# Optimization experiments

Measured on AMD Instinct MI355X. Metric: run time of the kernel, lower is better.

## Reference

```python
import jax, jax.numpy as jnp
import numpy as np

N_NODES = 50000
N_EDGES = 800000
IN_FEATS = 96
H_FEATS = 256
N_HOPS = 3
N_NIE = N_HOPS + 1  # hops 0..3
NDIM_FC = N_NIE * H_FEATS


def setup_inputs() -> dict:
    key = jax.random.key(0)
    ks = jax.random.split(key, 8)
    edge_index = jax.random.randint(ks[0], (2, N_EDGES), 0, N_NODES, dtype=jnp.int64)
    features = jax.random.normal(ks[1], (N_NODES, IN_FEATS), dtype=jnp.float32)
    # per-hop MLP params: Linear(in_feats, h_feats) for each of n_nie hops
    s_in = 1.0 / np.sqrt(IN_FEATS)
    Ws = jax.random.uniform(ks[2], (N_NIE, IN_FEATS, H_FEATS), jnp.float32, -s_in, s_in)
    bs = jax.random.uniform(ks[3], (N_NIE, H_FEATS), jnp.float32, -s_in, s_in)
    # fusion: Linear(ndim_fc, h_feats)
    s_fc = 1.0 / np.sqrt(NDIM_FC)
    Wf = jax.random.uniform(ks[4], (NDIM_FC, H_FEATS), jnp.float32, -s_fc, s_fc)
    bf = jax.random.uniform(ks[5], (H_FEATS,), jnp.float32, -s_fc, s_fc)
    return {"edge_index": edge_index, "features": features, "Ws": Ws, "bs": bs, "Wf": Wf, "bf": bf}


def _build_norm_adj(edge_index):
    """set_diag (remove existing diag, add unit self-loops) + symmetric D^-1/2 A D^-1/2.
    Returns (rows, cols, edge_w) COO of the normalized adjacency."""
    row, col = edge_index[0].astype(jnp.int32), edge_index[1].astype(jnp.int32)
    loop = jnp.arange(N_NODES, dtype=jnp.int32)
    rows = jnp.concatenate([row, loop])
    cols = jnp.concatenate([col, loop])
    # zero out any pre-existing diagonal entries, self-loops get weight 1 (set_diag semantics)
    w = jnp.concatenate([(row != col).astype(jnp.float32), jnp.ones((N_NODES,), jnp.float32)])
    deg = jax.ops.segment_sum(w, rows, num_segments=N_NODES)
    dinv = jnp.where(deg > 0, jax.lax.rsqrt(deg), 0.0)
    edge_w = dinv[rows] * w * dinv[cols]
    return rows, cols, edge_w


def _spmm(rows, cols, edge_w, x):
    # out[r] = sum_e w_e * x[cols[e]] for edges with rows[e]==r
    return jax.ops.segment_sum(edge_w[:, None] * x[cols], rows, num_segments=N_NODES)


def reference(edge_index, features, Ws, bs, Wf, bf):
    rows, cols, edge_w = _build_norm_adj(edge_index)
    # row-normalize features (F.normalize dim=1)
    x = features / jnp.maximum(jnp.linalg.norm(features, axis=1, keepdims=True), 1e-12)
    nei_feats = [x]
    h = x
    for _ in range(N_HOPS):
        h = _spmm(rows, cols, edge_w, h)
        nei_feats.append(h)
    # per-hop MLP (dropout p=0 -> identity; norm=None -> identity) then ReLU
    ns = [jax.nn.relu(nei_feats[i] @ Ws[i] + bs[i]) for i in range(N_NIE)]
    cat = jnp.concatenate(ns, axis=1)  # [N, ndim_fc]
    out = jax.nn.relu(cat @ Wf + bf)   # [N, h_feats]
    return out
```

## Files before the change

kernel.cpp:

```cpp
#include <hip/hip_runtime.h>

#define N_NODES 50000
#define N_EDGES 800000
#define IN_F 96
#define H_F 256
#define N_NIE 4
#define SCAN_NB 196
#define BM 64
#define NBLK 782
#define LDA1 104
#define LDW 40

typedef float f32x4 __attribute__((ext_vector_type(4)));
typedef short s16x8 __attribute__((ext_vector_type(8)));
typedef unsigned short ushort;

__device__ __forceinline__ ushort bf16_rne(float f) {
    unsigned u = __float_as_uint(f);
    u += 0x7fffu + ((u >> 16) & 1u);
    return (ushort)(u >> 16);
}
__device__ __forceinline__ float bf16_f(ushort h) {
    return __uint_as_float(((unsigned)h) << 16);
}

__global__ __launch_bounds__(256) void k_count(const int* __restrict__ rows,
                                               const int* __restrict__ cols,
                                               int* __restrict__ cnt) {
    int i = blockIdx.x * 256 + threadIdx.x;
    if (i >= N_EDGES / 2) return;
    int2 r2 = ((const int2*)rows)[i];
    int2 c2 = ((const int2*)cols)[i];
    if (r2.x != c2.x) atomicAdd(&cnt[r2.x], 1);
    if (r2.y != c2.y) atomicAdd(&cnt[r2.y], 1);
}

__global__ __launch_bounds__(256) void k_scan1(const int* __restrict__ cnt,
                                               int* __restrict__ rowptr,
                                               int* __restrict__ bsum) {
    __shared__ int s[256];
    int t = threadIdx.x, e = blockIdx.x * 256 + t;
    int v = (e < N_NODES) ? cnt[e] : 0;
    s[t] = v;
    __syncthreads();
    #pragma unroll
    for (int off = 1; off < 256; off <<= 1) {
        int nv = (t >= off) ? s[t - off] : 0;
        __syncthreads();
        s[t] += nv;
        __syncthreads();
    }
    if (e < N_NODES) rowptr[e] = s[t] - v;
    if (t == 255) bsum[blockIdx.x] = s[255];
}

__global__ __launch_bounds__(256) void k_scan2(int* __restrict__ bsum,
                                               int* __restrict__ boff,
                                               int* __restrict__ rowptr) {
    __shared__ int s[256];
    int t = threadIdx.x;
    int v = (t < SCAN_NB) ? bsum[t] : 0;
    s[t] = v;
    __syncthreads();
    #pragma unroll
    for (int off = 1; off < 256; off <<= 1) {
        int nv = (t >= off) ? s[t - off] : 0;
        __syncthreads();
        s[t] += nv;
        __syncthreads();
    }
    if (t < SCAN_NB) boff[t] = s[t] - v;
    if (t == 255) rowptr[N_NODES] = s[255];
}

__global__ __launch_bounds__(256) void k_scan3(const int* __restrict__ boff,
                                               const int* __restrict__ cnt,
                                               int* __restrict__ rowptr,
                                               int* __restrict__ cursor,
                                               float* __restrict__ dinv) {
    int e = blockIdx.x * 256 + threadIdx.x;
    if (e >= N_NODES) return;
    int r = rowptr[e] + boff[blockIdx.x];
    rowptr[e] = r;
    cursor[e] = r;
    dinv[e] = rsqrtf((float)cnt[e] + 1.0f);
}

__global__ __launch_bounds__(256) void k_scatter(const int* __restrict__ rows,
                                                 const int* __restrict__ cols,
                                                 const float* __restrict__ dinv,
                                                 int* __restrict__ cursor,
                                                 int2* __restrict__ cw) {
    int e = blockIdx.x * 256 + threadIdx.x;
    if (e >= N_EDGES) return;
    int r = rows[e], c = cols[e];
    if (r == c) return;
    int p = atomicAdd(&cursor[r], 1);
    long long v = ((long long)(unsigned)__float_as_int(dinv[c]) << 32) | (unsigned)c;
    __builtin_nontemporal_store(v, (long long*)&cw[p]);
}

__global__ __launch_bounds__(256) void k_wsplit(const float* __restrict__ src,
                                                ushort* __restrict__ dh,
                                                int K, int N, int total) {
    int idx = blockIdx.x * 256 + threadIdx.x;
    if (idx >= total) return;
    int kn = K * N;
    int g = idx / kn, rem = idx - g * kn;
    int k = rem / N, n = rem - k * N;
    dh[g * kn + n * K + k] = bf16_rne(src[idx]);
}

__global__ __launch_bounds__(256) void k_norm(const float* __restrict__ feat,
                                              ushort* __restrict__ x) {
    int wid = (blockIdx.x * 256 + threadIdx.x) >> 6;
    int lane = threadIdx.x & 63;
    if (wid >= N_NODES) return;
    const float* fr = feat + (size_t)wid * IN_F;
    float v0 = (lane < IN_F) ? fr[lane] : 0.0f;
    float v1 = (lane < IN_F - 64) ? fr[64 + lane] : 0.0f;
    float ss = v0 * v0 + v1 * v1;
    #pragma unroll
    for (int o = 32; o; o >>= 1) ss += __shfl_xor(ss, o, 64);
    float inv = 1.0f / fmaxf(sqrtf(ss), 1e-12f);
    ushort* xr = x + (size_t)wid * IN_F;
    if (lane < IN_F) xr[lane] = bf16_rne(v0 * inv);
    if (lane < IN_F - 64) xr[64 + lane] = bf16_rne(v1 * inv);
}

__global__ __launch_bounds__(256) void k_spmm_csr(const int* __restrict__ rowptr,
                                                  const int2* __restrict__ cw,
                                                  const float* __restrict__ dinv,
                                                  const ushort* __restrict__ x,
                                                  ushort* __restrict__ y) {
    int g = (blockIdx.x * 256 + threadIdx.x) >> 5;
    if (g >= N_NODES) return;
    int l = threadIdx.x & 31;
    float dr = dinv[g];
    const ushort* xg = x + (size_t)g * IN_F;
    float s0 = bf16_f(xg[l]), s1 = bf16_f(xg[l + 32]), s2 = bf16_f(xg[l + 64]);
    float a0 = 0.f, a1 = 0.f, a2 = 0.f;
    float b0 = 0.f, b1 = 0.f, b2 = 0.f;
    float c0 = 0.f, c1 = 0.f, c2 = 0.f;
    float d0 = 0.f, d1 = 0.f, d2 = 0.f;
    int k = rowptr[g], e = rowptr[g + 1];
    for (; k + 3 < e; k += 4) {
        int2 p0 = cw[k], p1 = cw[k + 1], p2 = cw[k + 2], p3 = cw[k + 3];
        const ushort* x0 = x + (size_t)p0.x * IN_F;
        const ushort* x1 = x + (size_t)p1.x * IN_F;
        const ushort* x2 = x + (size_t)p2.x * IN_F;
        const ushort* x3 = x + (size_t)p3.x * IN_F;
        float w0 = __int_as_float(p0.y), w1 = __int_as_float(p1.y);
        float w2 = __int_as_float(p2.y), w3 = __int_as_float(p3.y);
        a0 += bf16_f(x0[l]) * w0; a1 += bf16_f(x0[l + 32]) * w0; a2 += bf16_f(x0[l + 64]) * w0;
        b0 += bf16_f(x1[l]) * w1; b1 += bf16_f(x1[l + 32]) * w1; b2 += bf16_f(x1[l + 64]) * w1;
        c0 += bf16_f(x2[l]) * w2; c1 += bf16_f(x2[l + 32]) * w2; c2 += bf16_f(x2[l + 64]) * w2;
        d0 += bf16_f(x3[l]) * w3; d1 += bf16_f(x3[l + 32]) * w3; d2 += bf16_f(x3[l + 64]) * w3;
    }
    for (; k < e; ++k) {
        int2 p0 = cw[k];
        float w0 = __int_as_float(p0.y);
        const ushort* x0 = x + (size_t)p0.x * IN_F;
        a0 += bf16_f(x0[l]) * w0; a1 += bf16_f(x0[l + 32]) * w0; a2 += bf16_f(x0[l + 64]) * w0;
    }
    ushort* yr = y + (size_t)g * IN_F;
    yr[l]      = bf16_rne(dr * ((a0 + b0) + (c0 + d0) + dr * s0));
    yr[l + 32] = bf16_rne(dr * ((a1 + b1) + (c1 + d1) + dr * s1));
    yr[l + 64] = bf16_rne(dr * ((a2 + b2) + (c2 + d2) + dr * s2));
}

__global__ __launch_bounds__(512, 4) void k_mega(const ushort* __restrict__ h0,
                                                 const ushort* __restrict__ h1,
                                                 const ushort* __restrict__ h2,
                                                 const ushort* __restrict__ h3,
                                                 const ushort* __restrict__ WsT,
                                                 const float* __restrict__ bs,
                                                 const ushort* __restrict__ WfT,
                                                 const float* __restrict__ bf,
                                                 float* __restrict__ out) {
    __shared__ ushort SM[36864];
    ushort* nsH = SM;
    ushort* Wb0 = SM + 16384;
    ushort* Wb1 = SM + 26624;
    ushort* Bs = Wb0;
    ushort* Ah = Wb1;
    float* T = (float*)SM;

    int m0 = blockIdx.x * BM;
    int tid = threadIdx.x;
    int lane = tid & 63, w = tid >> 6;
    int rsel = lane & 15, g = lane >> 4, ksel = g * 8;
    int crow = g * 4, ccol = rsel;
    int rw0 = (w & 3) * 16;
    int cwb = (w >> 2) * 32;

    int sr0 = tid / 12, sj0 = tid - sr0 * 12;
    int f1 = tid + 512;
    int sr1 = f1 / 12, sj1 = f1 - sr1 * 12;
    int wr_ = tid >> 2, wj_ = tid & 3;

    f32x4 acc[4][2] = {};

    for (int hop = 0; hop < N_NIE; ++hop) {
        const ushort* A = (hop == 0) ? h0 : (hop == 1) ? h1 : (hop == 2) ? h2 : h3;
        const ushort* wsT = WsT + hop * IN_F * H_F;
        const ushort* wfT = WfT + hop * H_F * H_F;
        const float* bsi = bs + hop * H_F;

        {
            int gm = m0 + sr0;
            s16x8 v = {0, 0, 0, 0, 0, 0, 0, 0};
            if (gm < N_NODES) v = *(const s16x8*)&A[(size_t)gm * IN_F + sj0 * 8];
            *(s16x8*)&Ah[sr0 * LDA1 + sj0 * 8] = v;
            if (tid < 256) {
                int gm1 = m0 + sr1;
                s16x8 v1 = {0, 0, 0, 0, 0, 0, 0, 0};
                if (gm1 < N_NODES) v1 = *(const s16x8*)&A[(size_t)gm1 * IN_F + sj1 * 8];
                *(s16x8*)&Ah[sr1 * LDA1 + sj1 * 8] = v1;
            }
        }
        s16x8 breg0 = *(const s16x8*)&wsT[(size_t)sr0 * IN_F + sj0 * 8];
        s16x8 breg1 = {0, 0, 0, 0, 0, 0, 0, 0};
        if (tid < 256) breg1 = *(const s16x8*)&wsT[(size_t)sr1 * IN_F + sj1 * 8];
        s16x8 wrA[2], wrB[2];
        #pragma unroll
        for (int c = 0; c < 4; ++c) {
            __syncthreads();
            *(s16x8*)&Bs[sr0 * LDA1 + sj0 * 8] = breg0;
            if (tid < 256) *(s16x8*)&Bs[sr1 * LDA1 + sj1 * 8] = breg1;
            __syncthreads();
            if (c < 3) {
                const ushort* src = wsT + (size_t)(c + 1) * 64 * IN_F;
                breg0 = *(const s16x8*)&src[(size_t)sr0 * IN_F + sj0 * 8];
                if (tid < 256) breg1 = *(const s16x8*)&src[(size_t)sr1 * IN_F + sj1 * 8];
            } else {
                #pragma unroll
                for (int p = 0; p < 2; ++p) {
                    wrA[p] = *(const s16x8*)&wfT[(size_t)((tid + p * 512) >> 2) * H_F +
                                                 ((tid + p * 512) & 3) * 8];
                    wrB[p] = *(const s16x8*)&wfT[(size_t)((tid + p * 512) >> 2) * H_F + 32 +
                                                 ((tid + p * 512) & 3) * 8];
                }
            }
            f32x4 ac[2] = {};
            #pragma unroll
            for (int ks = 0; ks < 3; ++ks) {
                int k0 = ks * 32 + ksel;
                s16x8 ah = *(const s16x8*)&Ah[(rw0 + rsel) * LDA1 + k0];
                s16x8 b0 = *(const s16x8*)&Bs[(cwb + rsel) * LDA1 + k0];
                s16x8 b1 = *(const s16x8*)&Bs[(cwb + 16 + rsel) * LDA1 + k0];
                ac[0] = __builtin_amdgcn_mfma_f32_16x16x32_bf16(ah, b0, ac[0], 0, 0, 0);
                ac[1] = __builtin_amdgcn_mfma_f32_16x16x32_bf16(ah, b1, ac[1], 0, 0, 0);
            }
            #pragma unroll
            for (int cf = 0; cf < 2; ++cf) {
                int col = c * 64 + cwb + cf * 16 + ccol;
                float bb = bsi[col];
                #pragma unroll
                for (int ii = 0; ii < 4; ++ii) {
                    int row = rw0 + crow + ii;
                    nsH[row * 256 + (col ^ ((row & 7) << 3))] =
                        bf16_rne(fmaxf(ac[cf][ii] + bb, 0.f));
                }
            }
        }
        __syncthreads();
        #pragma unroll
        for (int kc2 = 0; kc2 < 4; ++kc2) {
            *(s16x8*)&Wb0[wr_ * LDW + wj_ * 8] = wrA[0];
            *(s16x8*)&Wb0[(wr_ + 128) * LDW + wj_ * 8] = wrA[1];
            __syncthreads();
            if (kc2 < 3) {
                #pragma unroll
                for (int p = 0; p < 2; ++p)
                    wrA[p] = *(const s16x8*)&wfT[(size_t)((tid + p * 512) >> 2) * H_F +
                                                 (2 * kc2 + 2) * 32 +
                                                 ((tid + p * 512) & 3) * 8];
            }
            {
                int k0 = (2 * kc2) * 32 + ksel;
                s16x8 ah4[4];
                #pragma unroll
                for (int rf = 0; rf < 4; ++rf) {
                    int row = rf * 16 + rsel;
                    ah4[rf] = *(const s16x8*)&nsH[row * 256 + (k0 ^ ((row & 7) << 3))];
                }
                #pragma unroll
                for (int cf = 0; cf < 2; ++cf) {
                    s16x8 bh = *(const s16x8*)&Wb0[(w * 32 + cf * 16 + rsel) * LDW + ksel];
                    #pragma unroll
                    for (int rf = 0; rf < 4; ++rf)
                        acc[rf][cf] = __builtin_amdgcn_mfma_f32_16x16x32_bf16(ah4[rf], bh, acc[rf][cf], 0, 0, 0);
                }
            }
            *(s16x8*)&Wb1[wr_ * LDW + wj_ * 8] = wrB[0];
            *(s16x8*)&Wb1[(wr_ + 128) * LDW + wj_ * 8] = wrB[1];
            __syncthreads();
            if (kc2 < 3) {
                #pragma unroll
                for (int p = 0; p < 2; ++p)
                    wrB[p] = *(const s16x8*)&wfT[(size_t)((tid + p * 512) >> 2) * H_F +
                                                 (2 * kc2 + 3) * 32 +
                                                 ((tid + p * 512) & 3) * 8];
            }
            {
                int k0 = (2 * kc2 + 1) * 32 + ksel;
                s16x8 ah4[4];
                #pragma unroll
                for (int rf = 0; rf < 4; ++rf) {
                    int row = rf * 16 + rsel;
                    ah4[rf] = *(const s16x8*)&nsH[row * 256 + (k0 ^ ((row & 7) << 3))];
                }
                #pragma unroll
                for (int cf = 0; cf < 2; ++cf) {
                    s16x8 bh = *(const s16x8*)&Wb1[(w * 32 + cf * 16 + rsel) * LDW + ksel];
                    #pragma unroll
                    for (int rf = 0; rf < 4; ++rf)
                        acc[rf][cf] = __builtin_amdgcn_mfma_f32_16x16x32_bf16(ah4[rf], bh, acc[rf][cf], 0, 0, 0);
                }
            }
            __syncthreads();
        }
    }
    #pragma unroll
    for (int half = 0; half < 2; ++half) {
        __syncthreads();
        #pragma unroll
        for (int rf2 = 0; rf2 < 2; ++rf2) {
            int rf = half * 2 + rf2;
            #pragma unroll
            for (int cf = 0; cf < 2; ++cf) {
                int col = w * 32 + cf * 16 + ccol;
                #pragma unroll
                for (int ii = 0; ii < 4; ++ii)
                    T[(rf2 * 16 + crow + ii) * 260 + col] = acc[rf][cf][ii];
            }
        }
        __syncthreads();
        #pragma unroll
        for (int p = 0; p < 4; ++p) {
            int flat = tid + p * 512;
            int r = flat >> 6, jc = flat & 63;
            int gm = m0 + half * 32 + r;
            if (gm < N_NODES) {
                f32x4 v = *(f32x4*)&T[r * 260 + jc * 4];
                f32x4 bb = *(const f32x4*)&bf[jc * 4];
                f32x4 o;
                #pragma unroll
                for (int q = 0; q < 4; ++q) o[q] = fmaxf(v[q] + bb[q], 0.f);
                *(f32x4*)&out[(size_t)gm * H_F + jc * 4] = o;
            }
        }
    }
}

extern "C" void kernel_launch(void* const* d_in, const int* in_sizes, int n_in,
                              void* d_out, int out_size, void* d_ws, size_t ws_size,
                              hipStream_t stream) {
    const int* ei = (const int*)d_in[0];
    const int* rows = ei;
    const int* cols = ei + N_EDGES;
    const float* feat = (const float*)d_in[1];
    const float* Ws = (const float*)d_in[2];
    const float* bs = (const float*)d_in[3];
    const float* Wf = (const float*)d_in[4];
    const float* bf = (const float*)d_in[5];
    float* out = (float*)d_out;

    ushort* h0 = (ushort*)d_ws;
    ushort* h1 = h0 + (size_t)N_NODES * IN_F;
    ushort* h2 = h1 + (size_t)N_NODES * IN_F;
    ushort* h3 = h2 + (size_t)N_NODES * IN_F;
    ushort* WsT = h3 + (size_t)N_NODES * IN_F;
    ushort* WfT = WsT + N_NIE * IN_F * H_F;
    float* dinv = (float*)(WfT + N_NIE * H_F * H_F);
    int* rowptr = (int*)(dinv + N_NODES);
    int* bsum = rowptr + 50004;
    int* boff = bsum + 256;
    int2* cw = (int2*)(boff + 256);
    int* cnt = (int*)h1;
    int* cursor = cnt + N_NODES;

    hipMemsetAsync(cnt, 0, N_NODES * sizeof(int), stream);
    k_count<<<(N_EDGES / 2 + 255) / 256, 256, 0, stream>>>(rows, cols, cnt);
    k_scan1<<<SCAN_NB, 256, 0, stream>>>(cnt, rowptr, bsum);
    k_scan2<<<1, 256, 0, stream>>>(bsum, boff, rowptr);
    k_scan3<<<SCAN_NB, 256, 0, stream>>>(boff, cnt, rowptr, cursor, dinv);
    k_scatter<<<(N_EDGES + 255) / 256, 256, 0, stream>>>(rows, cols, dinv, cursor, cw);
    k_wsplit<<<(N_NIE * IN_F * H_F + 255) / 256, 256, 0, stream>>>(Ws, WsT, IN_F, H_F,
                                                                   N_NIE * IN_F * H_F);
    k_wsplit<<<(N_NIE * H_F * H_F + 255) / 256, 256, 0, stream>>>(Wf, WfT, H_F, H_F,
                                                                  N_NIE * H_F * H_F);
    k_norm<<<(N_NODES + 3) / 4, 256, 0, stream>>>(feat, h0);

    k_spmm_csr<<<(N_NODES * 32 + 255) / 256, 256, 0, stream>>>(rowptr, cw, dinv, h0, h1);
    k_spmm_csr<<<(N_NODES * 32 + 255) / 256, 256, 0, stream>>>(rowptr, cw, dinv, h1, h2);
    k_spmm_csr<<<(N_NODES * 32 + 255) / 256, 256, 0, stream>>>(rowptr, cw, dinv, h2, h3);
    k_mega<<<NBLK, 512, 0, stream>>>(h0, h1, h2, h3, WsT, bs, WfT, bf, out);
}
```

Baseline: 300.9 us.

## Pre-swizzle weights into MFMA fragment order and load B operands directly from global

The weight preprocessing kernels now write Ws and Wf in the exact per-lane MFMA B-fragment order, so the fused MLP kernel reads B operands straight from global/L2 with one coalesced 16-byte load per lane. This removes the LDS staging of weight tiles and most of the __syncthreads barriers in the hop loop, and cuts shared memory from about 72KB to 45KB. Launch bounds are raised to 6 blocks per CU to use that room for occupancy. The trade-off is that every block re-reads weights from L2 instead of sharing them through LDS, and the loads lose the explicit register prefetch pipelining.

Measured after the change: 383.6 us. 27.5% more time.

```diff
diff --git a/kernel.cpp b/kernel.cpp
--- a/kernel.cpp
+++ b/kernel.cpp
@@ -9,7 +9,6 @@
 #define BM 64
 #define NBLK 782
 #define LDA1 104
-#define LDW 40
 
 typedef float f32x4 __attribute__((ext_vector_type(4)));
 typedef short s16x8 __attribute__((ext_vector_type(8)));
@@ -100,15 +99,31 @@
     __builtin_nontemporal_store(v, (long long*)&cw[p]);
 }
 
-__global__ __launch_bounds__(256) void k_wsplit(const float* __restrict__ src,
-                                                ushort* __restrict__ dh,
-                                                int K, int N, int total) {
+__global__ __launch_bounds__(256) void k_wsplit_ws(const float* __restrict__ src,
+                                                   ushort* __restrict__ dst) {
     int idx = blockIdx.x * 256 + threadIdx.x;
-    if (idx >= total) return;
-    int kn = K * N;
-    int g = idx / kn, rem = idx - g * kn;
-    int k = rem / N, n = rem - k * N;
-    dh[g * kn + n * K + k] = bf16_rne(src[idx]);
+    if (idx >= N_NIE * IN_F * H_F) return;
+    int hop = idx / (IN_F * H_F), rem = idx % (IN_F * H_F);
+    int k = rem / H_F, n = rem % H_F;
+    int c = n >> 6, wc = (n >> 5) & 1, b = (n >> 4) & 1, rsel = n & 15;
+    int ks = k >> 5, kk = k & 31;
+    int lane = (kk >> 3) * 16 + rsel, sel8 = kk & 7;
+    int d = (((((hop * 4 + c) * 2 + wc) * 2 + b) * 3 + ks) * 64 + lane) * 8 + sel8;
+    dst[d] = bf16_rne(src[idx]);
+}
+
+__global__ __launch_bounds__(256) void k_wsplit_wf(const float* __restrict__ src,
+                                                   ushort* __restrict__ dst) {
+    int idx = blockIdx.x * 256 + threadIdx.x;
+    if (idx >= N_NIE * H_F * H_F) return;
+    int hop = idx / (H_F * H_F), rem = idx % (H_F * H_F);
+    int k = rem / H_F, n = rem % H_F;
+    int kc = k >> 5, kk = k & 31;
+    int w = n >> 5, rem2 = n & 31;
+    int cf = rem2 >> 4, rsel = rem2 & 15;
+    int lane = (kk >> 3) * 16 + rsel, sel8 = kk & 7;
+    int d = ((((hop * 8 + kc) * 8 + w) * 2 + cf) * 64 + lane) * 8 + sel8;
+    dst[d] = bf16_rne(src[idx]);
 }
 
 __global__ __launch_bounds__(256) void k_norm(const float* __restrict__ feat,
@@ -169,21 +184,18 @@
     yr[l + 64] = bf16_rne(dr * ((a2 + b2) + (c2 + d2) + dr * s2));
 }
 
-__global__ __launch_bounds__(512, 4) void k_mega(const ushort* __restrict__ h0,
+__global__ __launch_bounds__(512, 6) void k_mega(const ushort* __restrict__ h0,
                                                  const ushort* __restrict__ h1,
                                                  const ushort* __restrict__ h2,
                                                  const ushort* __restrict__ h3,
-                                                 const ushort* __restrict__ WsT,
+                                                 const ushort* __restrict__ Ws2,
                                                  const float* __restrict__ bs,
-                                                 const ushort* __restrict__ WfT,
+                                                 const ushort* __restrict__ Wf2,
                                                  const float* __restrict__ bf,
                                                  float* __restrict__ out) {
-    __shared__ ushort SM[36864];
+    __shared__ ushort SM[23040];
     ushort* nsH = SM;
-    ushort* Wb0 = SM + 16384;
-    ushort* Wb1 = SM + 26624;
-    ushort* Bs = Wb0;
-    ushort* Ah = Wb1;
+    ushort* Ah  = SM + 16384;
     float* T = (float*)SM;
 
     int m0 = blockIdx.x * BM;
@@ -192,19 +204,19 @@
     int rsel = lane & 15, g = lane >> 4, ksel = g * 8;
     int crow = g * 4, ccol = rsel;
     int rw0 = (w & 3) * 16;
-    int cwb = (w >> 2) * 32;
+    int wc = w >> 2;
+    int cwb = wc * 32;
 
     int sr0 = tid / 12, sj0 = tid - sr0 * 12;
     int f1 = tid + 512;
     int sr1 = f1 / 12, sj1 = f1 - sr1 * 12;
-    int wr_ = tid >> 2, wj_ = tid & 3;
 
     f32x4 acc[4][2] = {};
 
     for (int hop = 0; hop < N_NIE; ++hop) {
         const ushort* A = (hop == 0) ? h0 : (hop == 1) ? h1 : (hop == 2) ? h2 : h3;
-        const ushort* wsT = WsT + hop * IN_F * H_F;
-        const ushort* wfT = WfT + hop * H_F * H_F;
+        const ushort* wsF = Ws2 + (size_t)hop * IN_F * H_F;
+        const ushort* wfF = Wf2 + (size_t)hop * H_F * H_F;
         const float* bsi = bs + hop * H_F;
 
         {
@@ -219,36 +231,16 @@
                 *(s16x8*)&Ah[sr1 * LDA1 + sj1 * 8] = v1;
             }
         }
-        s16x8 breg0 = *(const s16x8*)&wsT[(size_t)sr0 * IN_F + sj0 * 8];
-        s16x8 breg1 = {0, 0, 0, 0, 0, 0, 0, 0};
-        if (tid < 256) breg1 = *(const s16x8*)&wsT[(size_t)sr1 * IN_F + sj1 * 8];
-        s16x8 wrA[2], wrB[2];
+        __syncthreads();
         #pragma unroll
         for (int c = 0; c < 4; ++c) {
-            __syncthreads();
-            *(s16x8*)&Bs[sr0 * LDA1 + sj0 * 8] = breg0;
-            if (tid < 256) *(s16x8*)&Bs[sr1 * LDA1 + sj1 * 8] = breg1;
-            __syncthreads();
-            if (c < 3) {
-                const ushort* src = wsT + (size_t)(c + 1) * 64 * IN_F;
-                breg0 = *(const s16x8*)&src[(size_t)sr0 * IN_F + sj0 * 8];
-                if (tid < 256) breg1 = *(const s16x8*)&src[(size_t)sr1 * IN_F + sj1 * 8];
-            } else {
-                #pragma unroll
-                for (int p = 0; p < 2; ++p) {
-                    wrA[p] = *(const s16x8*)&wfT[(size_t)((tid + p * 512) >> 2) * H_F +
-                                                 ((tid + p * 512) & 3) * 8];
-                    wrB[p] = *(const s16x8*)&wfT[(size_t)((tid + p * 512) >> 2) * H_F + 32 +
-                                                 ((tid + p * 512) & 3) * 8];
-                }
-            }
+            const ushort* bsrc = wsF + (size_t)((c * 2 + wc) * 2) * 3 * 64 * 8;
             f32x4 ac[2] = {};
             #pragma unroll
             for (int ks = 0; ks < 3; ++ks) {
-                int k0 = ks * 32 + ksel;
-                s16x8 ah = *(const s16x8*)&Ah[(rw0 + rsel) * LDA1 + k0];
-                s16x8 b0 = *(const s16x8*)&Bs[(cwb + rsel) * LDA1 + k0];
-                s16x8 b1 = *(const s16x8*)&Bs[(cwb + 16 + rsel) * LDA1 + k0];
+                s16x8 ah = *(const s16x8*)&Ah[(rw0 + rsel) * LDA1 + ks * 32 + ksel];
+                s16x8 b0 = *(const s16x8*)&bsrc[(size_t)(ks * 64 + lane) * 8];
+                s16x8 b1 = *(const s16x8*)&bsrc[(size_t)((3 + ks) * 64 + lane) * 8];
                 ac[0] = __builtin_amdgcn_mfma_f32_16x16x32_bf16(ah, b0, ac[0], 0, 0, 0);
                 ac[1] = __builtin_amdgcn_mfma_f32_16x16x32_bf16(ah, b1, ac[1], 0, 0, 0);
             }
@@ -266,61 +258,23 @@
         }
         __syncthreads();
         #pragma unroll
-        for (int kc2 = 0; kc2 < 4; ++kc2) {
-            *(s16x8*)&Wb0[wr_ * LDW + wj_ * 8] = wrA[0];
-            *(s16x8*)&Wb0[(wr_ + 128) * LDW + wj_ * 8] = wrA[1];
-            __syncthreads();
-            if (kc2 < 3) {
+        for (int kc = 0; kc < 8; ++kc) {
+            int k0 = kc * 32 + ksel;
+            s16x8 ah4[4];
+            #pragma unroll
+            for (int rf = 0; rf < 4; ++rf) {
+                int row = rf * 16 + rsel;
+                ah4[rf] = *(const s16x8*)&nsH[row * 256 + (k0 ^ ((row & 7) << 3))];
+            }
+            #pragma unroll
+            for (int cf = 0; cf < 2; ++cf) {
+                s16x8 bh = *(const s16x8*)&wfF[(size_t)(((kc * 8 + w) * 2 + cf) * 64 + lane) * 8];
                 #pragma unroll
-                for (int p = 0; p < 2; ++p)
-                    wrA[p] = *(const s16x8*)&wfT[(size_t)((tid + p * 512) >> 2) * H_F +
-                                                 (2 * kc2 + 2) * 32 +
-                                                 ((tid + p * 512) & 3) * 8];
-            }
-            {
-                int k0 = (2 * kc2) * 32 + ksel;
-                s16x8 ah4[4];
-                #pragma unroll
-                for (int rf = 0; rf < 4; ++rf) {
-                    int row = rf * 16 + rsel;
-                    ah4[rf] = *(const s16x8*)&nsH[row * 256 + (k0 ^ ((row & 7) << 3))];
-                }
-                #pragma unroll
-                for (int cf = 0; cf < 2; ++cf) {
-                    s16x8 bh = *(const s16x8*)&Wb0[(w * 32 + cf * 16 + rsel) * LDW + ksel];
-                    #pragma unroll
-                    for (int rf = 0; rf < 4; ++rf)
-                        acc[rf][cf] = __builtin_amdgcn_mfma_f32_16x16x32_bf16(ah4[rf], bh, acc[rf][cf], 0, 0, 0);
-                }
-            }
-            *(s16x8*)&Wb1[wr_ * LDW + wj_ * 8] = wrB[0];
-            *(s16x8*)&Wb1[(wr_ + 128) * LDW + wj_ * 8] = wrB[1];
-            __syncthreads();
-            if (kc2 < 3) {
-                #pragma unroll
-                for (int p = 0; p < 2; ++p)
-                    wrB[p] = *(const s16x8*)&wfT[(size_t)((tid + p * 512) >> 2) * H_F +
-                                                 (2 * kc2 + 3) * 32 +
-                                                 ((tid + p * 512) & 3) * 8];
-            }
-            {
-                int k0 = (2 * kc2 + 1) * 32 + ksel;
-                s16x8 ah4[4];
-                #pragma unroll
-                for (int rf = 0; rf < 4; ++rf) {
-                    int row = rf * 16 + rsel;
-                    ah4[rf] = *(const s16x8*)&nsH[row * 256 + (k0 ^ ((row & 7) << 3))];
-                }
-                #pragma unroll
-                for (int cf = 0; cf < 2; ++cf) {
-                    s16x8 bh = *(const s16x8*)&Wb1[(w * 32 + cf * 16 + rsel) * LDW + ksel];
-                    #pragma unroll
-                    for (int rf = 0; rf < 4; ++rf)
-                        acc[rf][cf] = __builtin_amdgcn_mfma_f32_16x16x32_bf16(ah4[rf], bh, acc[rf][cf], 0, 0, 0);
-                }
-            }
-            __syncthreads();
-        }
+                for (int rf = 0; rf < 4; ++rf)
+                    acc[rf][cf] = __builtin_amdgcn_mfma_f32_16x16x32_bf16(ah4[rf], bh, acc[rf][cf], 0, 0, 0);
+            }
+        }
+        __syncthreads();
     }
     #pragma unroll
     for (int half = 0; half < 2; ++half) {
@@ -371,9 +325,9 @@
     ushort* h1 = h0 + (size_t)N_NODES * IN_F;
     ushort* h2 = h1 + (size_t)N_NODES * IN_F;
     ushort* h3 = h2 + (size_t)N_NODES * IN_F;
-    ushort* WsT = h3 + (size_t)N_NODES * IN_F;
-    ushort* WfT = WsT + N_NIE * IN_F * H_F;
-    float* dinv = (float*)(WfT + N_NIE * H_F * H_F);
+    ushort* Ws2 = h3 + (size_t)N_NODES * IN_F;
+    ushort* Wf2 = Ws2 + N_NIE * IN_F * H_F;
+    float* dinv = (float*)(Wf2 + N_NIE * H_F * H_F);
     int* rowptr = (int*)(dinv + N_NODES);
     int* bsum = rowptr + 50004;
     int* boff = bsum + 256;
@@ -387,14 +341,12 @@
     k_scan2<<<1, 256, 0, stream>>>(bsum, boff, rowptr);
     k_scan3<<<SCAN_NB, 256, 0, stream>>>(boff, cnt, rowptr, cursor, dinv);
     k_scatter<<<(N_EDGES + 255) / 256, 256, 0, stream>>>(rows, cols, dinv, cursor, cw);
-    k_wsplit<<<(N_NIE * IN_F * H_F + 255) / 256, 256, 0, stream>>>(Ws, WsT, IN_F, H_F,
-                                                                   N_NIE * IN_F * H_F);
-    k_wsplit<<<(N_NIE * H_F * H_F + 255) / 256, 256, 0, stream>>>(Wf, WfT, H_F, H_F,
-                                                                  N_NIE * H_F * H_F);
+    k_wsplit_ws<<<(N_NIE * IN_F * H_F + 255) / 256, 256, 0, stream>>>(Ws, Ws2);
+    k_wsplit_wf<<<(N_NIE * H_F * H_F + 255) / 256, 256, 0, stream>>>(Wf, Wf2);
     k_norm<<<(N_NODES + 3) / 4, 256, 0, stream>>>(feat, h0);
 
     k_spmm_csr<<<(N_NODES * 32 + 255) / 256, 256, 0, stream>>>(rowptr, cw, dinv, h0, h1);
     k_spmm_csr<<<(N_NODES * 32 + 255) / 256, 256, 0, stream>>>(rowptr, cw, dinv, h1, h2);
     k_spmm_csr<<<(N_NODES * 32 + 255) / 256, 256, 0, stream>>>(rowptr, cw, dinv, h2, h3);
-    k_mega<<<NBLK, 512, 0, stream>>>(h0, h1, h2, h3, WsT, bs, WfT, bf, out);
-}
+    k_mega<<<NBLK, 512, 0, stream>>>(h0, h1, h2, h3, Ws2, bs, Wf2, bf, out);
+}
```
